# Performance work log

Hardware: AMD Instinct MI355X
Metric: run time of the kernel (lower is better)

The kernel has to match this reference:

```python
import jax, jax.numpy as jnp
import numpy as np

EMBED_DIM = 2048
Q_HEADS = 32
KV_HEADS = 8
HEAD_DIM = EMBED_DIM // Q_HEADS  # 64
REPEATS = Q_HEADS // KV_HEADS    # 4


def setup_inputs() -> dict:
    key = jax.random.key(0)
    ks = jax.random.split(key, 5)
    B, T = 2, 2048
    x = jax.random.normal(ks[0], (B, T, EMBED_DIM), dtype=jnp.float32)
    s = 1.0 / np.sqrt(EMBED_DIM)
    # torch nn.Linear weights are [out_features, in_features]
    Wq = jax.random.uniform(ks[1], (Q_HEADS * HEAD_DIM, EMBED_DIM), minval=-s, maxval=s, dtype=jnp.float32)
    Wk = jax.random.uniform(ks[2], (KV_HEADS * HEAD_DIM, EMBED_DIM), minval=-s, maxval=s, dtype=jnp.float32)
    Wv = jax.random.uniform(ks[3], (KV_HEADS * HEAD_DIM, EMBED_DIM), minval=-s, maxval=s, dtype=jnp.float32)
    Wo = jax.random.uniform(ks[4], (EMBED_DIM, Q_HEADS * HEAD_DIM), minval=-s, maxval=s, dtype=jnp.float32)
    return {"x": x, "Wq": Wq, "Wk": Wk, "Wv": Wv, "Wo": Wo}


def reference(x, Wq, Wk, Wv, Wo):
    B, T, C = x.shape
    # projections (x @ W.T), then split heads
    q = (x @ Wq.T).reshape(B, T, Q_HEADS, HEAD_DIM)
    k = (x @ Wk.T).reshape(B, T, KV_HEADS, HEAD_DIM)
    v = (x @ Wv.T).reshape(B, T, KV_HEADS, HEAD_DIM)
    # group query heads by shared kv head: [B, kvH, rep, T, d]
    q = q.transpose(0, 2, 1, 3).reshape(B, KV_HEADS, REPEATS, T, HEAD_DIM)
    k = k.transpose(0, 2, 1, 3)  # [B, kvH, T, d]
    v = v.transpose(0, 2, 1, 3)
    scale = 1.0 / np.sqrt(HEAD_DIM)
    # scores: [B, kvH, rep, Tq, Tk] -- KV shared across rep (no materialized repeat)
    scores = jnp.einsum('bgrtd,bgsd->bgrts', q, k) * scale
    causal = jnp.tril(jnp.ones((T, T), dtype=bool))
    scores = jnp.where(causal, scores, jnp.finfo(scores.dtype).min)
    attn = jax.nn.softmax(scores, axis=-1)
    y = jnp.einsum('bgrts,bgsd->bgrtd', attn, v)
    # [B, kvH, rep, T, d] -> [B, T, qH*d]
    y = y.reshape(B, Q_HEADS, T, HEAD_DIM).transpose(0, 2, 1, 3).reshape(B, T, Q_HEADS * HEAD_DIM)
    return y @ Wo.T
```

## Files before the change

### kernel.cpp

```cpp
#include <hip/hip_runtime.h>

#define BATCH 2
#define SEQ   2048
#define CDIM  2048
#define QH    32
#define KVH   8
#define HD    64

typedef __bf16 bf16x8 __attribute__((ext_vector_type(8)));
typedef float  f32x4  __attribute__((ext_vector_type(4)));
typedef float  f32x16 __attribute__((ext_vector_type(16)));
typedef unsigned int u32;

#define GAS __attribute__((address_space(1)))
#define LAS __attribute__((address_space(3)))

__device__ __forceinline__ void gload_lds16(const void* g, void* l) {
  __builtin_amdgcn_global_load_lds((const GAS void*)g, (LAS void*)l, 16, 0, 0);
}

__device__ __forceinline__ unsigned short f2bf(float f) {
  union { float fv; unsigned u; } v; v.fv = f;
  unsigned r = v.u + 0x7FFF + ((v.u >> 16) & 1);
  return (unsigned short)(r >> 16);
}

__device__ __forceinline__ float fastexp2(float x) {
#if __has_builtin(__builtin_amdgcn_exp2f)
  return __builtin_amdgcn_exp2f(x);
#else
  return exp2f(x);
#endif
}

__device__ __forceinline__ u32 cvtpk_bf16(float lo, float hi) {
  u32 r;
  asm("v_cvt_pk_bf16_f32 %0, %1, %2" : "=v"(r) : "v"(lo), "v"(hi));
  return r;
}

__device__ __forceinline__ void permswap(u32& a, u32& b) {
  asm volatile("v_permlane32_swap_b32 %0, %1" : "+v"(a), "+v"(b));
}

__global__ __launch_bounds__(256) void cvt_all(
    const float* __restrict__ x,  const float* __restrict__ wq,
    const float* __restrict__ wk, const float* __restrict__ wv,
    const float* __restrict__ wo,
    unsigned short* __restrict__ xb,  unsigned short* __restrict__ wqb,
    unsigned short* __restrict__ wkb, unsigned short* __restrict__ wvb,
    unsigned short* __restrict__ wob)
{
  const int i = blockIdx.x * 256 + threadIdx.x;
  const float* s; unsigned short* d; int o;
  if      (i < 1048576) { s = x;  d = xb;  o = i; }
  else if (i < 1572864) { s = wq; d = wqb; o = i - 1048576; }
  else if (i < 1703936) { s = wk; d = wkb; o = i - 1572864; }
  else if (i < 1835008) { s = wv; d = wvb; o = i - 1703936; }
  else                  { s = wo; d = wob; o = i - 1835008; }
  const f32x4* sp = (const f32x4*)(s + (long)o * 8);
  f32x4 a = sp[0], b = sp[1];
  union { unsigned short u[8]; bf16x8 v; } ov;
  #pragma unroll
  for (int j = 0; j < 4; j++) { ov.u[j] = f2bf(a[j]); ov.u[4 + j] = f2bf(b[j]); }
  *(bf16x8*)(d + (long)o * 8) = ov.v;
}


__global__ __launch_bounds__(512, 2) void gemm_qkv(
    const unsigned short* __restrict__ A,
    const unsigned short* __restrict__ W0,
    const unsigned short* __restrict__ W1,
    const unsigned short* __restrict__ W2,
    unsigned short* __restrict__ O0,
    unsigned short* __restrict__ O1,
    unsigned short* __restrict__ O2)
{
  __shared__ unsigned short lds[65536];
  constexpr int K  = CDIM;
  constexpr int NT = K / 64;
  const int tid  = threadIdx.x;
  const int lane = tid & 63;
  const int l15  = lane & 15;
  const int lg   = lane >> 4;
  const int wid  = tid >> 6;
  const int wm   = wid >> 2;
  const int wn   = wid & 3;
  const int m0 = blockIdx.y * 256;
  const int n0 = blockIdx.x * 256;

  const unsigned short* Wp; int wrow0;
  if (n0 < 2048)      { Wp = W0; wrow0 = n0; }
  else if (n0 < 2560) { Wp = W1; wrow0 = n0 - 2048; }
  else                { Wp = W2; wrow0 = n0 - 2560; }

  const unsigned short* Ag = A  + (long)m0 * K;
  const unsigned short* Bg = Wp + (long)wrow0 * K;

  const int srow  = tid >> 3;
  const int scol8 = 8 * ((tid & 7) ^ (srow & 7));
  const int rswz  = (l15 & 7) << 3;

  f32x4 acc[8][4] = {};
  bf16x8 a[4][2], b[2][2];

#define STAGE(H, T)                                                           \
  do {                                                                        \
    const unsigned short* _s = ((H) < 2) ? Ag : Bg;                           \
    const int _rb = ((H) & 1) * 128 + srow;                                   \
    unsigned short* _d = &lds[((((T) & 1) << 2) + (H)) * 8192 + tid * 8];     \
    gload_lds16(_s + (long)_rb * K + (T) * 64 + scol8, _d);                   \
    gload_lds16(_s + (long)(_rb + 64) * K + (T) * 64 + scol8, _d + 4096);     \
  } while (0)

#define LDA(MH)                                                               \
  _Pragma("unroll") for (int _mi = 0; _mi < 4; _mi++)                         \
  _Pragma("unroll") for (int _kk = 0; _kk < 2; _kk++) {                       \
    const int _row = wm * 64 + _mi * 16 + l15;                                \
    const int _ce = (_kk * 32 + lg * 8) ^ rswz;                               \
    a[_mi][_kk] = *(const bf16x8*)&lds[bufb + (MH) * 8192 + _row * 64 + _ce]; \
  }

#define LDB(NH)                                                               \
  _Pragma("unroll") for (int _ni = 0; _ni < 2; _ni++)                         \
  _Pragma("unroll") for (int _kk = 0; _kk < 2; _kk++) {                       \
    const int _row = wn * 32 + _ni * 16 + l15;                                \
    const int _ce = (_kk * 32 + lg * 8) ^ rswz;                               \
    b[_ni][_kk] = *(const bf16x8*)&lds[bufb + (2 + (NH)) * 8192 +             \
                                       _row * 64 + _ce];                      \
  }

#define MFMAQ(MH, NH)                                                         \
  do {                                                                        \
    __builtin_amdgcn_s_setprio(1);                                            \
    _Pragma("unroll") for (int _mi = 0; _mi < 4; _mi++)                       \
    _Pragma("unroll") for (int _ni = 0; _ni < 2; _ni++)                       \
    _Pragma("unroll") for (int _kk = 0; _kk < 2; _kk++)                       \
      acc[(MH) * 4 + _mi][(NH) * 2 + _ni] =                                   \
        __builtin_amdgcn_mfma_f32_16x16x32_bf16(                              \
          a[_mi][_kk], b[_ni][_kk],                                           \
          acc[(MH) * 4 + _mi][(NH) * 2 + _ni], 0, 0, 0);                      \
    __builtin_amdgcn_s_setprio(0);                                            \
  } while (0)

#define BAR()                                                                 \
  do { __builtin_amdgcn_sched_barrier(0); __builtin_amdgcn_s_barrier(); } while (0)

  STAGE(0, 0); STAGE(3, 0); STAGE(1, 0); STAGE(2, 0);
  STAGE(0, 1); STAGE(3, 1); STAGE(1, 1);
  asm volatile("s_waitcnt vmcnt(6)" ::: "memory");
  BAR();

  for (int t = 0; t < NT; t++) {
    const int bufb = (t & 1) * 32768;
    LDA(0); LDB(0);
    if (t + 1 < NT) STAGE(2, t + 1);
    BAR();
    if (t + 2 < NT) STAGE(0, t + 2);
    MFMAQ(0, 0);
    LDB(1);
    MFMAQ(0, 1);
    LDA(1);
    BAR();
    if (t + 2 < NT) { STAGE(3, t + 2); STAGE(1, t + 2); }
    MFMAQ(1, 1);
    LDB(0);
    MFMAQ(1, 0);
    if (t + 2 < NT) asm volatile("s_waitcnt vmcnt(6)" ::: "memory");
    else            asm volatile("s_waitcnt vmcnt(0)" ::: "memory");
    BAR();
  }
#undef STAGE
#undef LDA
#undef LDB
#undef MFMAQ

  const int bb = m0 >> 11, t0 = m0 & 2047;
  if (n0 < 2560) {
    #pragma unroll
    for (int mi = 0; mi < 8; mi++) {
      const int rbase = (mi >> 2) * 128 + wm * 64 + (mi & 3) * 16 + lg * 4;
      #pragma unroll
      for (int ni = 0; ni < 4; ni++) {
        const int cg = n0 + (ni >> 1) * 128 + wn * 32 + (ni & 1) * 16 + l15;
        #pragma unroll
        for (int r = 0; r < 4; r++) {
          const int tt = t0 + rbase + r;
          const unsigned short bv = f2bf(acc[mi][ni][r]);
          if (cg < 2048) {
            const int hh = cg >> 6, dd = cg & 63;
            O0[(((long)(bb * QH + hh)) * SEQ + tt) * HD + dd] = bv;
          } else {
            const int nn = cg - 2048; const int gg = nn >> 6, dd = nn & 63;
            O1[(((long)(bb * KVH + gg)) * SEQ + tt) * HD + dd] = bv;
          }
        }
      }
    }
  } else {
    char* ldsb = (char*)lds;
    #pragma unroll
    for (int mi = 0; mi < 8; mi++) {
      const int rg0 = (mi >> 2) * 128 + wm * 64 + (mi & 3) * 16 + lg * 4;
      #pragma unroll
      for (int ni = 0; ni < 4; ni++) {
        const int cgl = (ni >> 1) * 128 + wn * 32 + (ni & 1) * 16 + l15;
        uint2 pk;
        pk.x = cvtpk_bf16(acc[mi][ni][0], acc[mi][ni][1]);
        pk.y = cvtpk_bf16(acc[mi][ni][2], acc[mi][ni][3]);
        const int byte = cgl * 512 + ((rg0 * 2) ^ ((cgl & 31) << 4));
        *(uint2*)(ldsb + byte) = pk;
      }
    }
    __syncthreads();
    const int nn0 = n0 - 2560;
    #pragma unroll
    for (int it = 0; it < 16; it++) {
      const int cgl = it * 16 + (tid >> 5);
      const int tch = tid & 31;
      const int byte = cgl * 512 + ((tch * 16) ^ ((cgl & 31) << 4));
      uint4 vv = *(uint4*)(ldsb + byte);
      const int nn = nn0 + cgl; const int gg = nn >> 6, dd = nn & 63;
      *(uint4*)(O2 + (((long)(bb * KVH + gg)) * HD + dd) * SEQ + t0 + tch * 8) = vv;
    }
  }
#undef BAR
}

__global__ __launch_bounds__(512, 2) void gemm_wo(
    const unsigned short* __restrict__ A,
    const unsigned short* __restrict__ W0,
    float* __restrict__ Of)
{
  __shared__ unsigned short lds[49152];
  constexpr int K  = CDIM;
  constexpr int NT = K / 64;
  const int tid  = threadIdx.x;
  const int lane = tid & 63;
  const int l15  = lane & 15;
  const int lg   = lane >> 4;
  const int wid  = tid >> 6;
  const int wm   = wid >> 2;
  const int wn   = wid & 3;
  const int m0 = blockIdx.y * 256;
  const int n0 = blockIdx.x * 128;

  const unsigned short* Ag = A  + (long)m0 * K;
  const unsigned short* Bg = W0 + (long)n0 * K;

  const int srow  = tid >> 3;
  const int scol8 = 8 * ((tid & 7) ^ (srow & 7));
  const int rswz  = (l15 & 7) << 3;

  f32x4 acc[8][2] = {};
  bf16x8 a[4][2], b[2][2];

#define STAGEA(H, T)                                                          \
  do {                                                                        \
    const int _rb = (H) * 128 + srow;                                         \
    unsigned short* _d = &lds[((T) & 1) * 24576 + (H) * 8192 + tid * 8];      \
    gload_lds16(Ag + (long)_rb * K + (T) * 64 + scol8, _d);                   \
    gload_lds16(Ag + (long)(_rb + 64) * K + (T) * 64 + scol8, _d + 4096);     \
  } while (0)

#define STAGEB(T)                                                             \
  do {                                                                        \
    unsigned short* _d = &lds[((T) & 1) * 24576 + 16384 + tid * 8];           \
    gload_lds16(Bg + (long)srow * K + (T) * 64 + scol8, _d);                  \
    gload_lds16(Bg + (long)(srow + 64) * K + (T) * 64 + scol8, _d + 4096);    \
  } while (0)

#define LDA(MH)                                                               \
  _Pragma("unroll") for (int _mi = 0; _mi < 4; _mi++)                         \
  _Pragma("unroll") for (int _kk = 0; _kk < 2; _kk++) {                       \
    const int _row = wm * 64 + _mi * 16 + l15;                                \
    const int _ce = (_kk * 32 + lg * 8) ^ rswz;                               \
    a[_mi][_kk] = *(const bf16x8*)&lds[bufb + (MH) * 8192 + _row * 64 + _ce]; \
  }

#define LDBW()                                                                \
  _Pragma("unroll") for (int _ni = 0; _ni < 2; _ni++)                         \
  _Pragma("unroll") for (int _kk = 0; _kk < 2; _kk++) {                       \
    const int _row = wn * 32 + _ni * 16 + l15;                                \
    const int _ce = (_kk * 32 + lg * 8) ^ rswz;                               \
    b[_ni][_kk] = *(const bf16x8*)&lds[bufb + 16384 + _row * 64 + _ce];       \
  }

#define MFMAH(MH)                                                             \
  do {                                                                        \
    __builtin_amdgcn_s_setprio(1);                                            \
    _Pragma("unroll") for (int _mi = 0; _mi < 4; _mi++)                       \
    _Pragma("unroll") for (int _ni = 0; _ni < 2; _ni++)                       \
    _Pragma("unroll") for (int _kk = 0; _kk < 2; _kk++)                       \
      acc[(MH) * 4 + _mi][_ni] =                                              \
        __builtin_amdgcn_mfma_f32_16x16x32_bf16(                              \
          a[_mi][_kk], b[_ni][_kk], acc[(MH) * 4 + _mi][_ni], 0, 0, 0);       \
    __builtin_amdgcn_s_setprio(0);                                            \
  } while (0)

#define BAR()                                                                 \
  do { __builtin_amdgcn_sched_barrier(0); __builtin_amdgcn_s_barrier(); } while (0)

  STAGEA(0, 0); STAGEB(0); STAGEA(1, 0);
  STAGEA(0, 1); STAGEA(1, 1);
  asm volatile("s_waitcnt vmcnt(4)" ::: "memory");
  BAR();

  for (int t = 0; t < NT; t++) {
    const int bufb = (t & 1) * 24576;
    LDA(0); LDBW();
    if (t + 1 < NT) STAGEB(t + 1);
    BAR();
    if (t + 2 < NT) STAGEA(0, t + 2);
    MFMAH(0);
    LDA(1);
    BAR();
    if (t + 2 < NT) STAGEA(1, t + 2);
    MFMAH(1);
    if (t + 2 < NT) asm volatile("s_waitcnt vmcnt(4)" ::: "memory");
    else            asm volatile("s_waitcnt vmcnt(0)" ::: "memory");
    BAR();
  }
#undef STAGEA
#undef STAGEB
#undef LDA
#undef LDBW
#undef MFMAH
#undef BAR

  #pragma unroll
  for (int mi = 0; mi < 8; mi++) {
    const int rbase = m0 + (mi >> 2) * 128 + wm * 64 + (mi & 3) * 16 + lg * 4;
    #pragma unroll
    for (int ni = 0; ni < 2; ni++) {
      const int cg = n0 + wn * 32 + ni * 16 + l15;
      #pragma unroll
      for (int r = 0; r < 4; r++)
        Of[(long)(rbase + r) * 2048 + cg] = acc[mi][ni][r];
    }
  }
}

__global__ __launch_bounds__(256, 3) void attn_kernel(
    const unsigned short* __restrict__ q,
    const unsigned short* __restrict__ k,
    const unsigned short* __restrict__ vt,
    unsigned short* __restrict__ y)
{
  __shared__ unsigned short Ks[2][4096];
  __shared__ unsigned short Vs[2][4096];
  __shared__ unsigned short Ytile[4][32][72];
  const int tid  = threadIdx.x;
  const int lane = tid & 63;
  const int l31  = lane & 31;
  const int lg2  = lane >> 5;
  const int w    = tid >> 6;

  const int idx = blockIdx.x;
  const int r   = idx & 7;
  const int s   = idx >> 3;
  const int j   = 15 - (s >> 3);
  const int qs  = s & 7;
  const int c   = r + ((qs & 1) << 3);
  const int g   = c >> 1;
  const int b   = c & 1;
  const int h   = g * 4 + (qs >> 1);

  const unsigned short* kbase = k  + ((long)(b * KVH + g)) * SEQ * HD;
  const unsigned short* vbase = vt + ((long)(b * KVH + g)) * HD * SEQ;
  const float kscale = 0.125f * 1.44269504088896340736f;
  const int fswz = (l31 & 7) << 3;

#define STAGE(T, CUR)                                                          \
  do {                                                                         \
    const int _tk = (T) << 6;                                                  \
    _Pragma("unroll")                                                          \
    for (int _c = 0; _c < 2; _c++) {                                           \
      const int _idx = (w * 2 + _c) * 64 + lane;                               \
      const int _row = _idx >> 3;                                              \
      const int _sw  = ((_idx & 7) * 8) ^ ((_row & 7) << 3);                   \
      gload_lds16(kbase + (long)(_tk + _row) * HD + _sw, &Ks[CUR][_idx * 8]);  \
      gload_lds16(vbase + (long)_row * SEQ + _tk + _sw, &Vs[CUR][_idx * 8]);   \
    }                                                                          \
  } while (0)

#define STEP(T, CUR)                                                           \
  do {                                                                         \
    bf16x8 kf[8];                                                              \
    _Pragma("unroll")                                                          \
    for (int _j = 0; _j < 2; _j++)                                             \
      _Pragma("unroll")                                                        \
      for (int _dc = 0; _dc < 4; _dc++)                                        \
        kf[_j * 4 + _dc] = *(const bf16x8*)&Ks[CUR][(_j * 32 + l31) * 64 +     \
                               ((_dc * 16 + lg2 * 8) ^ fswz)];                 \
    f32x16 st0 = {}, st1 = {};                                                 \
    __builtin_amdgcn_s_setprio(1);                                             \
    _Pragma("unroll")                                                          \
    for (int _dc = 0; _dc < 4; _dc++) {                                        \
      st0 = __builtin_amdgcn_mfma_f32_32x32x16_bf16(kf[_dc],     qf[_dc], st0, 0, 0, 0); \
      st1 = __builtin_amdgcn_mfma_f32_32x32x16_bf16(kf[4 + _dc], qf[_dc], st1, 0, 0, 0); \
    }                                                                          \
    __builtin_amdgcn_s_setprio(0);                                             \
    float s2[32];                                                              \
    if ((T) == n64w - 1) {                                                     \
      const int _thr = mthr + l31;                                             \
      _Pragma("unroll")                                                        \
      for (int _r = 0; _r < 16; _r++) {                                        \
        const int _kl = (_r & 3) + 8 * (_r >> 2) + 4 * lg2;                    \
        s2[_r]      = (_kl      > _thr) ? -__builtin_inff() : st0[_r];         \
        s2[16 + _r] = (_kl + 32 > _thr) ? -__builtin_inff() : st1[_r];         \
      }                                                                        \
    } else {                                                                   \
      _Pragma("unroll")                                                        \
      for (int _r = 0; _r < 16; _r++) {                                        \
        s2[_r] = st0[_r]; s2[16 + _r] = st1[_r];                               \
      }                                                                        \
    }                                                                          \
    float _m16[16], _m8[8], _m4[4];                                            \
    _Pragma("unroll")                                                          \
    for (int _i = 0; _i < 16; _i++) _m16[_i] = fmaxf(s2[_i], s2[_i + 16]);     \
    _Pragma("unroll")                                                          \
    for (int _i = 0; _i < 8; _i++) _m8[_i] = fmaxf(_m16[_i], _m16[_i + 8]);    \
    _Pragma("unroll")                                                          \
    for (int _i = 0; _i < 4; _i++) _m4[_i] = fmaxf(_m8[_i], _m8[_i + 4]);      \
    float _pm = fmaxf(fmaxf(_m4[0], _m4[1]), fmaxf(_m4[2], _m4[3]));           \
    _pm = fmaxf(_pm, __shfl_xor(_pm, 32));                                     \
    if (!__all(_pm <= mrow + 44.3614195558f)) {                                \
      const float _fs = fastexp2((mrow - _pm) * kscale);                       \
      mrow = _pm; lrow *= _fs;                                                 \
      _Pragma("unroll")                                                        \
      for (int _r = 0; _r < 16; _r++) { yacc0[_r] *= _fs; yacc1[_r] *= _fs; }  \
    }                                                                          \
    const float _nc = mrow * kscale;                                           \
    _Pragma("unroll")                                                          \
    for (int _r = 0; _r < 32; _r++)                                            \
      s2[_r] = fastexp2(__builtin_fmaf(s2[_r], kscale, -_nc));                 \
    float _a16[16], _a8[8], _a4[4];                                            \
    _Pragma("unroll")                                                          \
    for (int _i = 0; _i < 16; _i++) _a16[_i] = s2[_i] + s2[_i + 16];           \
    _Pragma("unroll")                                                          \
    for (int _i = 0; _i < 8; _i++) _a8[_i] = _a16[_i] + _a16[_i + 8];          \
    _Pragma("unroll")                                                          \
    for (int _i = 0; _i < 4; _i++) _a4[_i] = _a8[_i] + _a8[_i + 4];            \
    float _sum = (_a4[0] + _a4[1]) + (_a4[2] + _a4[3]);                        \
    _sum += __shfl_xor(_sum, 32);                                              \
    lrow += _sum;                                                              \
    union { u32 u[4]; bf16x8 v; } _pb[4];                                      \
    _Pragma("unroll")                                                          \
    for (int _jj = 0; _jj < 2; _jj++) {                                        \
      const int _o = _jj * 16;                                                 \
      u32 _w0 = cvtpk_bf16(s2[_o + 0],  s2[_o + 1]);                           \
      u32 _w1 = cvtpk_bf16(s2[_o + 2],  s2[_o + 3]);                           \
      u32 _w2 = cvtpk_bf16(s2[_o + 4],  s2[_o + 5]);                           \
      u32 _w3 = cvtpk_bf16(s2[_o + 6],  s2[_o + 7]);                           \
      u32 _w4 = cvtpk_bf16(s2[_o + 8],  s2[_o + 9]);                           \
      u32 _w5 = cvtpk_bf16(s2[_o + 10], s2[_o + 11]);                          \
      u32 _w6 = cvtpk_bf16(s2[_o + 12], s2[_o + 13]);                          \
      u32 _w7 = cvtpk_bf16(s2[_o + 14], s2[_o + 15]);                          \
      permswap(_w0, _w2); permswap(_w1, _w3);                                  \
      permswap(_w4, _w6); permswap(_w5, _w7);                                  \
      _pb[_jj * 2].u[0] = _w0; _pb[_jj * 2].u[1] = _w1;                        \
      _pb[_jj * 2].u[2] = _w2; _pb[_jj * 2].u[3] = _w3;                        \
      _pb[_jj * 2 + 1].u[0] = _w4; _pb[_jj * 2 + 1].u[1] = _w5;                \
      _pb[_jj * 2 + 1].u[2] = _w6; _pb[_jj * 2 + 1].u[3] = _w7;                \
    }                                                                          \
    bf16x8 vf[8];                                                              \
    _Pragma("unroll")                                                          \
    for (int _c = 0; _c < 4; _c++) {                                           \
      vf[_c * 2]     = *(const bf16x8*)&Vs[CUR][l31 * 64 +                     \
                           ((_c * 16 + lg2 * 8) ^ fswz)];                      \
      vf[_c * 2 + 1] = *(const bf16x8*)&Vs[CUR][(32 + l31) * 64 +              \
                           ((_c * 16 + lg2 * 8) ^ fswz)];                      \
    }                                                                          \
    __builtin_amdgcn_s_setprio(1);                                             \
    _Pragma("unroll")                                                          \
    for (int _c = 0; _c < 4; _c++) {                                           \
      yacc0 = __builtin_amdgcn_mfma_f32_32x32x16_bf16(vf[_c * 2],     _pb[_c].v, yacc0, 0, 0, 0); \
      yacc1 = __builtin_amdgcn_mfma_f32_32x32x16_bf16(vf[_c * 2 + 1], _pb[_c].v, yacc1, 0, 0, 0); \
    }                                                                          \
    __builtin_amdgcn_s_setprio(0);                                             \
  } while (0)

  const int i      = 4 * j + w;
  const int q0     = i * 32;
  const int n64w   = (i >> 1) + 1;
  const int n64max = 2 * j + 2;
  const int mthr   = (i & 1) ? 32 : 0;
  const unsigned short* qbase = q + (((long)(b * QH + h)) * SEQ + q0) * HD;

  bf16x8 qf[4];
  #pragma unroll
  for (int dc = 0; dc < 4; dc++)
    qf[dc] = *(const bf16x8*)(qbase + (long)l31 * HD + dc * 16 + (lg2 << 3));

  float mrow = -__builtin_inff(), lrow = 0.f;
  f32x16 yacc0 = {}, yacc1 = {};

  STAGE(0, 0);
  int cur = 0;
  for (int t = 0; t < n64max; t++) {
    __syncthreads();
    if (t + 1 < n64max) STAGE(t + 1, cur ^ 1);
    if (t < n64w) STEP(t, cur);
    cur ^= 1;
  }

  const float rl = 1.f / lrow;
  #pragma unroll
  for (int r2 = 0; r2 < 16; r2++) {
    const int dv = (r2 & 3) + 8 * (r2 >> 2) + 4 * lg2;
    Ytile[w][l31][dv]      = f2bf(yacc0[r2] * rl);
    Ytile[w][l31][32 + dv] = f2bf(yacc1[r2] * rl);
  }
  asm volatile("s_waitcnt lgkmcnt(0)" ::: "memory");
  __builtin_amdgcn_sched_barrier(0);
  #pragma unroll
  for (int it = 0; it < 4; it++) {
    const int qr = it * 8 + (lane >> 3);
    const int dc = (lane & 7) * 8;
    bf16x8 vv = *(const bf16x8*)&Ytile[w][qr][dc];
    *(bf16x8*)(y + (((long)b * SEQ + q0 + qr) * QH + h) * HD + dc) = vv;
  }
#undef STAGE
#undef STEP
}

extern "C" void kernel_launch(void* const* d_in, const int* in_sizes, int n_in,
                              void* d_out, int out_size, void* d_ws, size_t ws_size,
                              hipStream_t stream) {
  const float* xf  = (const float*)d_in[0];
  const float* Wqf = (const float*)d_in[1];
  const float* Wkf = (const float*)d_in[2];
  const float* Wvf = (const float*)d_in[3];
  const float* Wof = (const float*)d_in[4];

  const int nx  = 8388608;
  const int nwq = 4194304;
  const int nwk = 1048576;
  const int nwv = 1048576;
  const int nwo = 4194304;

  unsigned short* ws  = (unsigned short*)d_ws;
  unsigned short* xb  = ws;
  unsigned short* Wqb = xb  + nx;
  unsigned short* Wkb = Wqb + nwq;
  unsigned short* Wvb = Wkb + nwk;
  unsigned short* Wob = Wvb + nwv;
  unsigned short* qb  = Wob + nwo;
  unsigned short* kb  = qb  + 8388608;
  unsigned short* vtb = kb  + 2097152;
  unsigned short* yb  = vtb + 2097152;
  float* ob = (float*)d_out;

  cvt_all<<<dim3(9216), dim3(256), 0, stream>>>(xf, Wqf, Wkf, Wvf, Wof,
                                                xb, Wqb, Wkb, Wvb, Wob);
  gemm_qkv<<<dim3(12, 16), dim3(512), 0, stream>>>(xb, Wqb, Wkb, Wvb, qb, kb, vtb);
  attn_kernel<<<dim3(1024), dim3(256), 0, stream>>>(qb, kb, vtb, yb);
  gemm_wo<<<dim3(16, 16), dim3(512), 0, stream>>>(yb, Wob, ob);
}
```

Measured before the change: 161.4 us.

## Retile fused QKV GEMM to 256x192 tiles for a 256-block grid

The QKV projection GEMM switches from 256x256 tiles on a 12x16 grid to 256x192 tiles on a 16x16 grid. It treats Wq/Wk/Wv as one contiguous weight matrix, which relies on the workspace placing them back to back. Tiles that straddle the K/V boundary now split their epilogue per column, with V written transposed through LDS. The goal is to fill all 256 compute units instead of 192 blocks leaving some idle. The cost is a smaller per-block tile with less reuse and a more branchy epilogue.

```diff
diff --git a/kernel.cpp b/kernel.cpp
--- a/kernel.cpp
+++ b/kernel.cpp
@@ -69,14 +69,12 @@
 
 __global__ __launch_bounds__(512, 2) void gemm_qkv(
     const unsigned short* __restrict__ A,
-    const unsigned short* __restrict__ W0,
-    const unsigned short* __restrict__ W1,
-    const unsigned short* __restrict__ W2,
+    const unsigned short* __restrict__ W,
     unsigned short* __restrict__ O0,
     unsigned short* __restrict__ O1,
     unsigned short* __restrict__ O2)
 {
-  __shared__ unsigned short lds[65536];
+  __shared__ unsigned short lds[57344];
   constexpr int K  = CDIM;
   constexpr int NT = K / 64;
   const int tid  = threadIdx.x;
@@ -84,143 +82,134 @@
   const int l15  = lane & 15;
   const int lg   = lane >> 4;
   const int wid  = tid >> 6;
-  const int wm   = wid >> 2;
-  const int wn   = wid & 3;
+  const int wm   = wid >> 1;
+  const int wn   = wid & 1;
   const int m0 = blockIdx.y * 256;
-  const int n0 = blockIdx.x * 256;
-
-  const unsigned short* Wp; int wrow0;
-  if (n0 < 2048)      { Wp = W0; wrow0 = n0; }
-  else if (n0 < 2560) { Wp = W1; wrow0 = n0 - 2048; }
-  else                { Wp = W2; wrow0 = n0 - 2560; }
-
-  const unsigned short* Ag = A  + (long)m0 * K;
-  const unsigned short* Bg = Wp + (long)wrow0 * K;
+  const int n0 = blockIdx.x * 192;
+
+  const unsigned short* Ag = A + (long)m0 * K;
+  const unsigned short* Bg = W + (long)n0 * K;
 
   const int srow  = tid >> 3;
   const int scol8 = 8 * ((tid & 7) ^ (srow & 7));
   const int rswz  = (l15 & 7) << 3;
 
-  f32x4 acc[8][4] = {};
-  bf16x8 a[4][2], b[2][2];
-
-#define STAGE(H, T)                                                           \
+  f32x4 acc[4][6] = {};
+  bf16x8 a[4][2], b[3][2];
+
+#define SA(T)                                                                 \
   do {                                                                        \
-    const unsigned short* _s = ((H) < 2) ? Ag : Bg;                           \
-    const int _rb = ((H) & 1) * 128 + srow;                                   \
-    unsigned short* _d = &lds[((((T) & 1) << 2) + (H)) * 8192 + tid * 8];     \
-    gload_lds16(_s + (long)_rb * K + (T) * 64 + scol8, _d);                   \
-    gload_lds16(_s + (long)(_rb + 64) * K + (T) * 64 + scol8, _d + 4096);     \
-  } while (0)
-
-#define LDA(MH)                                                               \
+    unsigned short* _d = &lds[(((T) & 1) * 28672) + tid * 8];                 \
+    _Pragma("unroll")                                                         \
+    for (int _pp = 0; _pp < 4; _pp++)                                         \
+      gload_lds16(Ag + (long)(_pp * 64 + srow) * K + (T) * 64 + scol8,        \
+                  _d + _pp * 4096);                                           \
+  } while (0)
+
+#define SB(T)                                                                 \
+  do {                                                                        \
+    unsigned short* _d = &lds[(((T) & 1) * 28672) + 16384 + tid * 8];         \
+    _Pragma("unroll")                                                         \
+    for (int _pp = 0; _pp < 3; _pp++)                                         \
+      gload_lds16(Bg + (long)(_pp * 64 + srow) * K + (T) * 64 + scol8,        \
+                  _d + _pp * 4096);                                           \
+  } while (0)
+
+#define LDA()                                                                 \
   _Pragma("unroll") for (int _mi = 0; _mi < 4; _mi++)                         \
   _Pragma("unroll") for (int _kk = 0; _kk < 2; _kk++) {                       \
     const int _row = wm * 64 + _mi * 16 + l15;                                \
     const int _ce = (_kk * 32 + lg * 8) ^ rswz;                               \
-    a[_mi][_kk] = *(const bf16x8*)&lds[bufb + (MH) * 8192 + _row * 64 + _ce]; \
+    a[_mi][_kk] = *(const bf16x8*)&lds[bufb + _row * 64 + _ce];               \
   }
 
 #define LDB(NH)                                                               \
-  _Pragma("unroll") for (int _ni = 0; _ni < 2; _ni++)                         \
+  _Pragma("unroll") for (int _ni = 0; _ni < 3; _ni++)                         \
   _Pragma("unroll") for (int _kk = 0; _kk < 2; _kk++) {                       \
-    const int _row = wn * 32 + _ni * 16 + l15;                                \
+    const int _row = wn * 96 + ((NH) * 3 + _ni) * 16 + l15;                   \
     const int _ce = (_kk * 32 + lg * 8) ^ rswz;                               \
-    b[_ni][_kk] = *(const bf16x8*)&lds[bufb + (2 + (NH)) * 8192 +             \
-                                       _row * 64 + _ce];                      \
-  }
-
-#define MFMAQ(MH, NH)                                                         \
+    b[_ni][_kk] = *(const bf16x8*)&lds[bufb + 16384 + _row * 64 + _ce];       \
+  }
+
+#define MFMAQ(NH)                                                             \
   do {                                                                        \
     __builtin_amdgcn_s_setprio(1);                                            \
     _Pragma("unroll") for (int _mi = 0; _mi < 4; _mi++)                       \
-    _Pragma("unroll") for (int _ni = 0; _ni < 2; _ni++)                       \
+    _Pragma("unroll") for (int _ni = 0; _ni < 3; _ni++)                       \
     _Pragma("unroll") for (int _kk = 0; _kk < 2; _kk++)                       \
-      acc[(MH) * 4 + _mi][(NH) * 2 + _ni] =                                   \
+      acc[_mi][(NH) * 3 + _ni] =                                              \
         __builtin_amdgcn_mfma_f32_16x16x32_bf16(                              \
-          a[_mi][_kk], b[_ni][_kk],                                           \
-          acc[(MH) * 4 + _mi][(NH) * 2 + _ni], 0, 0, 0);                      \
+          a[_mi][_kk], b[_ni][_kk], acc[_mi][(NH) * 3 + _ni], 0, 0, 0);       \
     __builtin_amdgcn_s_setprio(0);                                            \
   } while (0)
 
 #define BAR()                                                                 \
   do { __builtin_amdgcn_sched_barrier(0); __builtin_amdgcn_s_barrier(); } while (0)
 
-  STAGE(0, 0); STAGE(3, 0); STAGE(1, 0); STAGE(2, 0);
-  STAGE(0, 1); STAGE(3, 1); STAGE(1, 1);
-  asm volatile("s_waitcnt vmcnt(6)" ::: "memory");
+  SA(0); SB(0); SA(1);
+  asm volatile("s_waitcnt vmcnt(4)" ::: "memory");
   BAR();
 
   for (int t = 0; t < NT; t++) {
-    const int bufb = (t & 1) * 32768;
-    LDA(0); LDB(0);
-    if (t + 1 < NT) STAGE(2, t + 1);
+    const int bufb = (t & 1) * 28672;
+    if (t + 1 < NT) SB(t + 1);
+    LDA(); LDB(0);
     BAR();
-    if (t + 2 < NT) STAGE(0, t + 2);
-    MFMAQ(0, 0);
+    if (t + 2 < NT) SA(t + 2);
+    MFMAQ(0);
     LDB(1);
-    MFMAQ(0, 1);
-    LDA(1);
-    BAR();
-    if (t + 2 < NT) { STAGE(3, t + 2); STAGE(1, t + 2); }
-    MFMAQ(1, 1);
-    LDB(0);
-    MFMAQ(1, 0);
-    if (t + 2 < NT) asm volatile("s_waitcnt vmcnt(6)" ::: "memory");
+    MFMAQ(1);
+    if (t + 2 < NT) asm volatile("s_waitcnt vmcnt(4)" ::: "memory");
     else            asm volatile("s_waitcnt vmcnt(0)" ::: "memory");
     BAR();
   }
-#undef STAGE
+#undef SA
+#undef SB
 #undef LDA
 #undef LDB
 #undef MFMAQ
 
   const int bb = m0 >> 11, t0 = m0 & 2047;
-  if (n0 < 2560) {
+  const int vstart = (n0 > 2560) ? n0 : 2560;
+  const int nV = n0 + 192 - vstart;
+  char* ldsb = (char*)lds;
+  #pragma unroll
+  for (int mi = 0; mi < 4; mi++) {
+    const int rg0 = wm * 64 + mi * 16 + lg * 4;
     #pragma unroll
-    for (int mi = 0; mi < 8; mi++) {
-      const int rbase = (mi >> 2) * 128 + wm * 64 + (mi & 3) * 16 + lg * 4;
-      #pragma unroll
-      for (int ni = 0; ni < 4; ni++) {
-        const int cg = n0 + (ni >> 1) * 128 + wn * 32 + (ni & 1) * 16 + l15;
+    for (int ni = 0; ni < 6; ni++) {
+      const int cg = n0 + wn * 96 + ni * 16 + l15;
+      if (cg < 2048) {
+        const int hh = cg >> 6, dd = cg & 63;
         #pragma unroll
-        for (int r = 0; r < 4; r++) {
-          const int tt = t0 + rbase + r;
-          const unsigned short bv = f2bf(acc[mi][ni][r]);
-          if (cg < 2048) {
-            const int hh = cg >> 6, dd = cg & 63;
-            O0[(((long)(bb * QH + hh)) * SEQ + tt) * HD + dd] = bv;
-          } else {
-            const int nn = cg - 2048; const int gg = nn >> 6, dd = nn & 63;
-            O1[(((long)(bb * KVH + gg)) * SEQ + tt) * HD + dd] = bv;
-          }
-        }
-      }
-    }
-  } else {
-    char* ldsb = (char*)lds;
-    #pragma unroll
-    for (int mi = 0; mi < 8; mi++) {
-      const int rg0 = (mi >> 2) * 128 + wm * 64 + (mi & 3) * 16 + lg * 4;
-      #pragma unroll
-      for (int ni = 0; ni < 4; ni++) {
-        const int cgl = (ni >> 1) * 128 + wn * 32 + (ni & 1) * 16 + l15;
+        for (int r = 0; r < 4; r++)
+          O0[(((long)(bb * QH + hh)) * SEQ + t0 + rg0 + r) * HD + dd] =
+              f2bf(acc[mi][ni][r]);
+      } else if (cg < 2560) {
+        const int nn = cg - 2048, gg = nn >> 6, dd = nn & 63;
+        #pragma unroll
+        for (int r = 0; r < 4; r++)
+          O1[(((long)(bb * KVH + gg)) * SEQ + t0 + rg0 + r) * HD + dd] =
+              f2bf(acc[mi][ni][r]);
+      } else {
+        const int cglV = cg - vstart;
         uint2 pk;
         pk.x = cvtpk_bf16(acc[mi][ni][0], acc[mi][ni][1]);
         pk.y = cvtpk_bf16(acc[mi][ni][2], acc[mi][ni][3]);
-        const int byte = cgl * 512 + ((rg0 * 2) ^ ((cgl & 31) << 4));
+        const int byte = cglV * 512 + ((rg0 * 2) ^ ((cglV & 31) << 4));
         *(uint2*)(ldsb + byte) = pk;
       }
     }
+  }
+  if (nV > 0) {
     __syncthreads();
-    const int nn0 = n0 - 2560;
-    #pragma unroll
-    for (int it = 0; it < 16; it++) {
-      const int cgl = it * 16 + (tid >> 5);
+    const int nn0 = vstart - 2560;
+    for (int it = 0; it < nV / 16; it++) {
+      const int cglV = it * 16 + (tid >> 5);
       const int tch = tid & 31;
-      const int byte = cgl * 512 + ((tch * 16) ^ ((cgl & 31) << 4));
+      const int byte = cglV * 512 + ((tch * 16) ^ ((cglV & 31) << 4));
       uint4 vv = *(uint4*)(ldsb + byte);
-      const int nn = nn0 + cgl; const int gg = nn >> 6, dd = nn & 63;
+      const int nn = nn0 + cglV, gg = nn >> 6, dd = nn & 63;
       *(uint4*)(O2 + (((long)(bb * KVH + gg)) * HD + dd) * SEQ + t0 + tch * 8) = vv;
     }
   }
@@ -554,7 +543,7 @@
 
   cvt_all<<<dim3(9216), dim3(256), 0, stream>>>(xf, Wqf, Wkf, Wvf, Wof,
                                                 xb, Wqb, Wkb, Wvb, Wob);
-  gemm_qkv<<<dim3(12, 16), dim3(512), 0, stream>>>(xb, Wqb, Wkb, Wvb, qb, kb, vtb);
+  gemm_qkv<<<dim3(16, 16), dim3(512), 0, stream>>>(xb, Wqb, qb, kb, vtb);
   attn_kernel<<<dim3(1024), dim3(256), 0, stream>>>(qb, kb, vtb, yb);
   gemm_wo<<<dim3(16, 16), dim3(512), 0, stream>>>(yb, Wob, ob);
 }
```

Result: faster. 155.0 us (-3.9%).
